# Performance work log

Hardware: AMD Instinct MI355X
Metric: run time of the kernel (lower is better)

Reference implementation:

```python
import jax, jax.numpy as jnp
import numpy as np

N, E = 50000, 800000
IN_DIM, H, OUT = 16, 256, 64
L = 3
REL_DIM, ROLE_DIM, COL_DIM = 16, 8, 8
NUM_REL, NUM_ROLE, NUM_COL = 8, 8, 3
EDGE_IN = 2 * H + REL_DIM + 2 * ROLE_DIM + 2 * COL_DIM   # 560
NODE_IN = 2 * H + ROLE_DIM + COL_DIM                     # 528
LN_EPS = 1e-5


def setup_inputs() -> dict:
    key = jax.random.key(0)
    ks = jax.random.split(key, 32)
    s = 0.02
    inp = {
        "scalars": jax.random.normal(ks[0], (N, IN_DIM), jnp.float32),
        "edge_index": jax.random.randint(ks[1], (2, E), 0, N),
        "edge_relation": jax.random.randint(ks[2], (E,), 0, NUM_REL),
        "node_color_rep": jax.random.randint(ks[3], (N,), 0, NUM_COL),
        "node_role": jax.random.randint(ks[4], (N,), 0, NUM_ROLE),
        # block-level embeddings + input projection (weights stored [in,out])
        "blk_role_emb": jax.random.normal(ks[5], (NUM_ROLE, 8), jnp.float32) * s,
        "blk_color_emb": jax.random.normal(ks[6], (NUM_COL, 8), jnp.float32) * s,
        "in_w": jax.random.normal(ks[7], (IN_DIM + 16, H), jnp.float32) * s,
        "in_b": jnp.zeros((H,), jnp.float32),
        # per-layer params, stacked over L
        "rel_embs": jax.random.normal(ks[8], (L, NUM_REL, REL_DIM), jnp.float32) * s,
        "role_embs": jax.random.normal(ks[9], (L, NUM_ROLE, ROLE_DIM), jnp.float32) * s,
        "col_embs": jax.random.normal(ks[10], (L, NUM_COL, COL_DIM), jnp.float32) * s,
        "e1_w": jax.random.normal(ks[11], (L, EDGE_IN, H), jnp.float32) * s,
        "e1_b": jnp.zeros((L, H), jnp.float32),
        "e2_w": jax.random.normal(ks[12], (L, H, H), jnp.float32) * s,
        "e2_b": jnp.zeros((L, H), jnp.float32),
        "n1_w": jax.random.normal(ks[13], (L, NODE_IN, H), jnp.float32) * s,
        "n1_b": jnp.zeros((L, H), jnp.float32),
        "n2_w": jax.random.normal(ks[14], (L, H, H), jnp.float32) * s,
        "n2_b": jnp.zeros((L, H), jnp.float32),
        "ln_g": jnp.ones((L, H), jnp.float32),
        "ln_b": jnp.zeros((L, H), jnp.float32),
        "out_w": jax.random.normal(ks[15], (H, OUT), jnp.float32) * s,
        "out_b": jnp.zeros((OUT,), jnp.float32),
    }
    return inp


def _layer(h, edge_index, edge_relation, node_color_rep, node_role,
           rel_e, role_e, col_e, e1w, e1b, e2w, e2b, n1w, n1b, n2w, n2b, g, b):
    src, dst = edge_index[0], edge_index[1]
    role_all = role_e[node_role]           # [N, ROLE_DIM]
    col_all = col_e[node_color_rep]        # [N, COL_DIM]
    edge_in = jnp.concatenate(
        [h[src], h[dst], rel_e[edge_relation],
         role_all[src], role_all[dst], col_all[src], col_all[dst]], axis=-1)
    m = jax.nn.silu(edge_in @ e1w + e1b)
    m = jax.nn.silu(m @ e2w + e2b)                       # [E, H]
    agg = jax.ops.segment_sum(m, dst, num_segments=h.shape[0])
    node_in = jnp.concatenate([h, agg, role_all, col_all], axis=-1)
    upd = jax.nn.silu(node_in @ n1w + n1b) @ n2w + n2b
    x = h + upd
    mu = jnp.mean(x, axis=-1, keepdims=True)
    var = jnp.mean(jnp.square(x - mu), axis=-1, keepdims=True)
    return g * (x - mu) * jax.lax.rsqrt(var + LN_EPS) + b


def reference(scalars, edge_index, edge_relation, node_color_rep, node_role,
              blk_role_emb, blk_color_emb, in_w, in_b,
              rel_embs, role_embs, col_embs,
              e1_w, e1_b, e2_w, e2_b, n1_w, n1_b, n2_w, n2_b,
              ln_g, ln_b, out_w, out_b):
    node_in = jnp.concatenate(
        [scalars, blk_color_emb[node_color_rep], blk_role_emb[node_role]], axis=-1)
    h = node_in @ in_w + in_b
    for i in range(L):
        h = _layer(h, edge_index, edge_relation, node_color_rep, node_role,
                   rel_embs[i], role_embs[i], col_embs[i],
                   e1_w[i], e1_b[i], e2_w[i], e2_b[i],
                   n1_w[i], n1_b[i], n2_w[i], n2_b[i],
                   ln_g[i], ln_b[i])
    return h @ out_w + out_b
```

## Files before the change

### kernel.cpp

```cpp
#include <hip/hip_runtime.h>

#define NN 50000
#define NE 800000
#define H 256
#define NBINS 50176

typedef __bf16 bf16x8 __attribute__((ext_vector_type(8)));
typedef __bf16 bf16x4 __attribute__((ext_vector_type(4)));
typedef float f32x4 __attribute__((ext_vector_type(4)));

static __device__ __forceinline__ f32x4 mfma16(bf16x8 a, bf16x8 b, f32x4 c) {
  return __builtin_amdgcn_mfma_f32_16x16x32_bf16(a, b, c, 0, 0, 0);
}
static __device__ __forceinline__ bf16x8 bzero8() {
  bf16x8 z;
#pragma unroll
  for (int j = 0; j < 8; ++j) z[j] = (__bf16)0.f;
  return z;
}
static __device__ __forceinline__ float silu_f(float v) {
  return v * __builtin_amdgcn_rcpf(1.f + __builtin_amdgcn_exp2f(v * -1.442695041f));
}

__global__ void prep_kernel(
    const float* __restrict__ e1w, const float* __restrict__ e2w,
    const float* __restrict__ n1w, const float* __restrict__ n2w,
    const float* __restrict__ outw,
    __bf16* __restrict__ wsd, __bf16* __restrict__ e2p,
    __bf16* __restrict__ n1p, __bf16* __restrict__ n2p,
    __bf16* __restrict__ outp)
{
  int i = blockIdx.x * 256 + threadIdx.x;
  if (i < 3 * 131072) {
    const int l = i / 131072, rem = i % 131072;
    const int c = rem >> 14, r2 = rem & 16383;
    const int n = r2 >> 5, k = c * 32 + (r2 & 31);
    wsd[i] = (n < 256) ? (__bf16)e1w[((size_t)l * 560 + k) * 256 + n]
                       : (__bf16)e1w[((size_t)l * 560 + 256 + k) * 256 + (n - 256)];
    return;
  }
  i -= 3 * 131072;
  if (i < 3 * 8 * 8192) {
    const int l = i / 65536, rem = i % 65536;
    const int c = rem >> 13, r2 = rem & 8191;
    const int n = r2 >> 5, k = c * 32 + (r2 & 31);
    e2p[i] = (__bf16)e2w[((size_t)l * 256 + k) * 256 + n];
    return;
  }
  i -= 3 * 8 * 8192;
  if (i < 3 * 17 * 8192) {
    const int l = i / (17 * 8192), rem = i % (17 * 8192);
    const int c = rem >> 13, r2 = rem & 8191;
    const int n = r2 >> 5, k = c * 32 + (r2 & 31);
    n1p[i] = (k < 528) ? (__bf16)n1w[((size_t)l * 528 + k) * 256 + n] : (__bf16)0.f;
    return;
  }
  i -= 3 * 17 * 8192;
  if (i < 3 * 8 * 8192) {
    const int l = i / 65536, rem = i % 65536;
    const int c = rem >> 13, r2 = rem & 8191;
    const int n = r2 >> 5, k = c * 32 + (r2 & 31);
    n2p[i] = (__bf16)n2w[((size_t)l * 256 + k) * 256 + n];
    return;
  }
  i -= 3 * 8 * 8192;
  if (i < 8 * 2048) {
    const int c = i >> 11, r2 = i & 2047;
    const int n = r2 >> 5, k = c * 32 + (r2 & 31);
    outp[i] = (__bf16)outw[(size_t)k * 64 + n];
  }
}

__global__ __launch_bounds__(256) void tbl_kernel(
    const float* __restrict__ e1w, const float* __restrict__ e1b,
    const float* __restrict__ rel_embs, const float* __restrict__ role_embs,
    const float* __restrict__ col_embs,
    float* __restrict__ TR, float* __restrict__ TS, float* __restrict__ TD)
{
  const int l = blockIdx.x, c = threadIdx.x;
  float w[48];
#pragma unroll
  for (int j = 0; j < 48; ++j) w[j] = e1w[((size_t)l * 560 + 512 + j) * 256 + c];
#pragma unroll
  for (int r = 0; r < 8; ++r) {
    float s = 0.f;
#pragma unroll
    for (int j = 0; j < 16; ++j) s += rel_embs[l * 128 + r * 16 + j] * w[j];
    TR[((size_t)l * 8 + r) * 256 + c] = s;
  }
  const float bias = e1b[l * 256 + c];
#pragma unroll
  for (int ro = 0; ro < 8; ++ro) {
    float ss = 0.f, sd = 0.f;
#pragma unroll
    for (int j = 0; j < 8; ++j) {
      ss += role_embs[l * 64 + ro * 8 + j] * w[16 + j];
      sd += role_embs[l * 64 + ro * 8 + j] * w[24 + j];
    }
#pragma unroll
    for (int co = 0; co < 3; ++co) {
      float cs = 0.f, cd = 0.f;
#pragma unroll
      for (int j = 0; j < 8; ++j) {
        cs += col_embs[l * 24 + co * 8 + j] * w[32 + j];
        cd += col_embs[l * 24 + co * 8 + j] * w[40 + j];
      }
      TS[((size_t)l * 24 + ro * 3 + co) * 256 + c] = ss + cs;
      TD[((size_t)l * 24 + ro * 3 + co) * 256 + c] = sd + cd + bias;
    }
  }
}

__global__ void hist_kernel(const int* __restrict__ dstI, int* __restrict__ cnt) {
  const int e = blockIdx.x * 256 + threadIdx.x;
  if (e < NE) atomicAdd(&cnt[dstI[e]], 1);
}

__global__ __launch_bounds__(256) void scan_kernel(int* __restrict__ cnt) {
  __shared__ int wsum[4];
  __shared__ int sCarry;
  const int tid = threadIdx.x, lane = tid & 63, wid = tid >> 6;
  if (tid == 0) sCarry = 0;
  __syncthreads();
  for (int base = 0; base < NBINS; base += 256) {
    const int i = base + tid;
    const int v = cnt[i];
    int x = v;
#pragma unroll
    for (int d = 1; d < 64; d <<= 1) {
      const int y = __shfl_up(x, d, 64);
      if (lane >= d) x += y;
    }
    if (lane == 63) wsum[wid] = x;
    __syncthreads();
    int wpref = 0;
#pragma unroll
    for (int w = 0; w < 4; ++w)
      if (w < wid) wpref += wsum[w];
    cnt[i] = sCarry + wpref + x - v;
    __syncthreads();
    if (tid == 0) sCarry += wsum[0] + wsum[1] + wsum[2] + wsum[3];
    __syncthreads();
  }
}

__global__ void scatter_kernel(const int* __restrict__ srcI, const int* __restrict__ dstI,
                               const int* __restrict__ erel, int* __restrict__ cnt,
                               int* __restrict__ srcS, int* __restrict__ dstS,
                               int* __restrict__ relS) {
  const int e = blockIdx.x * 256 + threadIdx.x;
  if (e < NE) {
    const int d = dstI[e];
    const int pos = atomicAdd(&cnt[d], 1);
    srcS[pos] = srcI[e];
    dstS[pos] = d;
    relS[pos] = erel[e];
  }
}

__global__ __launch_bounds__(256) void embed_kernel(
    const float* __restrict__ scalars, const int* __restrict__ ncol,
    const int* __restrict__ nrole,
    const float* __restrict__ colEmb, const float* __restrict__ roleEmb,
    const float* __restrict__ inw, const float* __restrict__ inb,
    __bf16* __restrict__ h)
{
  __shared__ float sW[32][256];
  __shared__ float sIn[16][32];
  const int tid = threadIdx.x;
  const int n0 = blockIdx.x * 16;
#pragma unroll
  for (int j = 0; j < 32; ++j) sW[j][tid] = inw[j * 256 + tid];
  {
    const int node = tid >> 4, k = tid & 15;
    const int n = n0 + node;
    sIn[node][k] = (n < NN) ? scalars[(size_t)n * 16 + k] : 0.f;
  }
  if (tid < 16) {
    const int n = n0 + tid;
    if (n < NN) {
      const int c = ncol[n], r = nrole[n];
#pragma unroll
      for (int j = 0; j < 8; ++j) {
        sIn[tid][16 + j] = colEmb[c * 8 + j];
        sIn[tid][24 + j] = roleEmb[r * 8 + j];
      }
    } else {
#pragma unroll
      for (int j = 0; j < 16; ++j) sIn[tid][16 + j] = 0.f;
    }
  }
  __syncthreads();
  const float bias = inb[tid];
  for (int nn = 0; nn < 16; ++nn) {
    const int n = n0 + nn;
    if (n >= NN) break;
    float acc = bias;
#pragma unroll
    for (int k = 0; k < 32; ++k) acc += sIn[nn][k] * sW[k][tid];
    h[(size_t)n * H + tid] = (__bf16)acc;
  }
}

__global__ __launch_bounds__(256, 4) void pre_kernel(
    const __bf16* __restrict__ h, const int* __restrict__ nrole,
    const int* __restrict__ ncol, const __bf16* __restrict__ wsd,
    const float* __restrict__ TS, const float* __restrict__ TD,
    __bf16* __restrict__ PS, __bf16* __restrict__ PD)
{
  __shared__ __align__(16) __bf16 Ah[64][72];
  const int tid  = threadIdx.x;
  const int lane = tid & 63;
  const int wave = tid >> 6;
  const int l15  = lane & 15;
  const int quad = lane >> 4;
  const int n0   = (blockIdx.x >> 1) * 64;
  const int half = blockIdx.x & 1;
  const int colW = wave * 64;

  f32x4 acc[4][4] = {};
  for (int s = 0; s < 4; ++s) {
    if (s) __syncthreads();
#pragma unroll
    for (int it = 0; it < 2; ++it) {
      const int t = tid + it * 256;
      const int row = t >> 3, seg = t & 7;
      const int n = n0 + row;
      bf16x8 v = bzero8();
      if (n < NN) v = *(const bf16x8*)(h + (size_t)n * H + s * 64 + seg * 8);
      *(bf16x8*)&Ah[row][seg * 8] = v;
    }
    __syncthreads();
#pragma unroll
    for (int cc = 0; cc < 2; ++cc) {
      const int c = 2 * s + cc;
      bf16x8 bfr[4], afr[4];
#pragma unroll
      for (int nj = 0; nj < 4; ++nj)
        bfr[nj] = *(const bf16x8*)(wsd + ((size_t)c * 512 + half * 256 + colW + nj * 16 + l15) * 32 + quad * 8);
#pragma unroll
      for (int mi = 0; mi < 4; ++mi)
        afr[mi] = *(const bf16x8*)&Ah[mi * 16 + l15][cc * 32 + quad * 8];
#pragma unroll
      for (int mi = 0; mi < 4; ++mi)
#pragma unroll
        for (int nj = 0; nj < 4; ++nj)
          acc[mi][nj] = mfma16(afr[mi], bfr[nj], acc[mi][nj]);
    }
  }

  const float* T = half ? TD : TS;
  __bf16* P = half ? PD : PS;
#pragma unroll
  for (int mi = 0; mi < 4; ++mi)
#pragma unroll
    for (int r = 0; r < 4; ++r) {
      const int n = n0 + mi * 16 + quad * 4 + r;
      if (n < NN) {
        const int ti = (nrole[n] * 3 + ncol[n]) * 256;
#pragma unroll
        for (int nj = 0; nj < 4; ++nj) {
          const int col = colW + nj * 16 + l15;
          P[(size_t)n * H + col] = (__bf16)(acc[mi][nj][r] + T[ti + col]);
        }
      }
    }
}

__global__ __launch_bounds__(256, 4) void edge_kernel(
    const __bf16* __restrict__ PS, const __bf16* __restrict__ PD,
    float* __restrict__ agg,
    const int* __restrict__ srcS, const int* __restrict__ dstS,
    const int* __restrict__ relS, const float* __restrict__ TR,
    const __bf16* __restrict__ e2p, const float* __restrict__ e2b)
{
  __shared__ __align__(16) char uni[34816];
  __shared__ __bf16 sTrel[8][256];
  __shared__ int sSrc[64], sDst[64], sRel[64];
  __shared__ int sFlag[2];

  auto A2  = (__bf16 (*)[264])uni;
  auto A2t = (__bf16 (*)[68])uni;

  const int tid  = threadIdx.x;
  const int lane = tid & 63;
  const int wave = tid >> 6;
  const int l15  = lane & 15;
  const int quad = lane >> 4;
  const int e0   = blockIdx.x * 64;
  const int colW = wave * 64;

  if (tid < 64) {
    sSrc[tid] = srcS[e0 + tid];
    sDst[tid] = dstS[e0 + tid];
    sRel[tid] = relS[e0 + tid];
  }
  {
    const int r = tid >> 5, cs = (tid & 31) * 8;
    const float* p = TR + r * 256 + cs;
    bf16x8 v;
#pragma unroll
    for (int j = 0; j < 8; ++j) v[j] = (__bf16)p[j];
    *(bf16x8*)&sTrel[r][cs] = v;
  }
  if (tid == 0) sFlag[0] = (e0 > 0) && (dstS[e0 - 1] == dstS[e0]);
  if (tid == 1) sFlag[1] = (e0 + 64 < NE) && (dstS[e0 + 64] == dstS[e0 + 63]);
  __syncthreads();

  {
    const int brow = tid >> 5;
    const int cs = (tid & 31) * 8;
#pragma unroll
    for (int it = 0; it < 8; ++it) {
      const int row = it * 8 + brow;
      const bf16x8 a = *(const bf16x8*)(PS + (size_t)sSrc[row] * H + cs);
      const bf16x8 b = *(const bf16x8*)(PD + (size_t)sDst[row] * H + cs);
      const bf16x8 t = *(const bf16x8*)&sTrel[sRel[row]][cs];
      bf16x8 o;
#pragma unroll
      for (int j = 0; j < 8; ++j)
        o[j] = (__bf16)silu_f((float)a[j] + (float)b[j] + (float)t[j]);
      *(bf16x8*)&A2[row][cs] = o;
    }
  }
  __syncthreads();

  f32x4 acc2[4][4] = {};
#pragma unroll
  for (int c = 0; c < 8; ++c) {
    bf16x8 bfr[4], afr[4];
#pragma unroll
    for (int nj = 0; nj < 4; ++nj)
      bfr[nj] = *(const bf16x8*)(e2p + ((size_t)c * 256 + colW + nj * 16 + l15) * 32 + quad * 8);
#pragma unroll
    for (int mi = 0; mi < 4; ++mi)
      afr[mi] = *(const bf16x8*)&A2[mi * 16 + l15][c * 32 + quad * 8];
#pragma unroll
    for (int mi = 0; mi < 4; ++mi)
#pragma unroll
      for (int nj = 0; nj < 4; ++nj)
        acc2[mi][nj] = mfma16(afr[mi], bfr[nj], acc2[mi][nj]);
  }

  float b2[4];
#pragma unroll
  for (int nj = 0; nj < 4; ++nj) b2[nj] = e2b[colW + nj * 16 + l15];
  __syncthreads();

#pragma unroll
  for (int mi = 0; mi < 4; ++mi)
#pragma unroll
    for (int nj = 0; nj < 4; ++nj) {
      const int col = colW + nj * 16 + l15;
      bf16x4 pv;
#pragma unroll
      for (int r = 0; r < 4; ++r)
        pv[r] = (__bf16)silu_f(acc2[mi][nj][r] + b2[nj]);
      *(bf16x4*)&A2t[col][mi * 16 + quad * 4] = pv;
    }
  __syncthreads();

  {
    const int col = tid;
    const bool f = (lane > 0) && (sDst[lane] != sDst[lane - 1]);
    const unsigned long long mask = __ballot(f);
    const bool fF = sFlag[0] != 0, fL = sFlag[1] != 0;
    bf16x4 v[16];
#pragma unroll
    for (int j = 0; j < 16; ++j) v[j] = *(const bf16x4*)&A2t[col][j * 4];
    float sum = 0.f;
    int s0 = 0;
#pragma unroll
    for (int r = 0; r < 64; ++r) {
      sum += (float)v[r >> 2][r & 3];
      if (r == 63 || ((mask >> (r + 1)) & 1ull)) {
        float* addr = agg + (size_t)sDst[r] * H + col;
        const bool shared = (s0 == 0 && fF) || (r == 63 && fL);
        if (shared) atomicAdd(addr, sum);
        else *addr = sum;
        sum = 0.f;
        s0 = r + 1;
      }
    }
  }
}

__global__ __launch_bounds__(256, 4) void node_kernel(
    __bf16* __restrict__ h, const float* __restrict__ agg,
    const int* __restrict__ nrole, const int* __restrict__ ncol,
    const float* __restrict__ roleE, const float* __restrict__ colE,
    const __bf16* __restrict__ n1p, const float* __restrict__ n1b,
    const __bf16* __restrict__ n2p, const float* __restrict__ n2b,
    const float* __restrict__ lng, const float* __restrict__ lnb)
{
  __shared__ __align__(16) char uni[33792];
  __shared__ __bf16 sRole[8][8], sCol[3][8];
  __shared__ float sSum[64][4], sSsq[64][4];

  auto Abuf = (__bf16 (*)[72])uni;
  auto A2   = (__bf16 (*)[264])uni;

  const int tid  = threadIdx.x;
  const int lane = tid & 63;
  const int wave = tid >> 6;
  const int l15  = lane & 15;
  const int quad = lane >> 4;
  const int n0   = blockIdx.x * 64;
  const int colW = wave * 64;

  if (tid < 64) ((__bf16*)sRole)[tid] = (__bf16)roleE[tid];
  else if (tid < 88) ((__bf16*)sCol)[tid - 64] = (__bf16)colE[tid - 64];
  __syncthreads();

  f32x4 acc[4][4] = {};
  for (int s = 0; s < 9; ++s) {
    if (s) __syncthreads();
    if (s < 4) {
#pragma unroll
      for (int it = 0; it < 2; ++it) {
        const int t = tid + it * 256;
        const int row = t >> 3, seg = t & 7;
        const int n = n0 + row;
        bf16x8 v = bzero8();
        if (n < NN) v = *(const bf16x8*)(h + (size_t)n * H + s * 64 + seg * 8);
        *(bf16x8*)&Abuf[row][seg * 8] = v;
      }
    } else if (s < 8) {
#pragma unroll
      for (int it = 0; it < 2; ++it) {
        const int t = tid + it * 256;
        const int row = t >> 3, seg = t & 7;
        const int n = n0 + row;
        bf16x8 v = bzero8();
        if (n < NN) {
          const float* p = agg + (size_t)n * H + (s - 4) * 64 + seg * 8;
          const float4 u0 = *(const float4*)p;
          const float4 u1 = *(const float4*)(p + 4);
          v[0] = (__bf16)u0.x; v[1] = (__bf16)u0.y; v[2] = (__bf16)u0.z; v[3] = (__bf16)u0.w;
          v[4] = (__bf16)u1.x; v[5] = (__bf16)u1.y; v[6] = (__bf16)u1.z; v[7] = (__bf16)u1.w;
        }
        *(bf16x8*)&Abuf[row][seg * 8] = v;
      }
    } else {
      const int row = tid >> 2, q = tid & 3;
      const int n = n0 + row;
      __bf16* dp = &Abuf[row][q * 16];
      if (q == 0 && n < NN) {
        const int r = nrole[n], c = ncol[n];
#pragma unroll
        for (int j = 0; j < 8; ++j) { dp[j] = sRole[r][j]; dp[8 + j] = sCol[c][j]; }
      } else {
#pragma unroll
        for (int j = 0; j < 16; ++j) dp[j] = (__bf16)0.f;
      }
    }
    __syncthreads();
#pragma unroll
    for (int cc = 0; cc < 2; ++cc) {
      const int c = 2 * s + cc;
      if (c >= 17) break;
      bf16x8 bfr[4], afr[4];
#pragma unroll
      for (int nj = 0; nj < 4; ++nj)
        bfr[nj] = *(const bf16x8*)(n1p + ((size_t)c * 256 + colW + nj * 16 + l15) * 32 + quad * 8);
#pragma unroll
      for (int mi = 0; mi < 4; ++mi)
        afr[mi] = *(const bf16x8*)&Abuf[mi * 16 + l15][cc * 32 + quad * 8];
#pragma unroll
      for (int mi = 0; mi < 4; ++mi)
#pragma unroll
        for (int nj = 0; nj < 4; ++nj)
          acc[mi][nj] = mfma16(afr[mi], bfr[nj], acc[mi][nj]);
    }
  }
  __syncthreads();

  float b1[4];
#pragma unroll
  for (int nj = 0; nj < 4; ++nj) b1[nj] = n1b[colW + nj * 16 + l15];
#pragma unroll
  for (int mi = 0; mi < 4; ++mi)
#pragma unroll
    for (int nj = 0; nj < 4; ++nj)
#pragma unroll
      for (int r = 0; r < 4; ++r)
        A2[mi * 16 + quad * 4 + r][colW + nj * 16 + l15] =
            (__bf16)silu_f(acc[mi][nj][r] + b1[nj]);
  __syncthreads();

  f32x4 acc2[4][4] = {};
#pragma unroll
  for (int c = 0; c < 8; ++c) {
    bf16x8 bfr[4], afr[4];
#pragma unroll
    for (int nj = 0; nj < 4; ++nj)
      bfr[nj] = *(const bf16x8*)(n2p + ((size_t)c * 256 + colW + nj * 16 + l15) * 32 + quad * 8);
#pragma unroll
    for (int mi = 0; mi < 4; ++mi)
      afr[mi] = *(const bf16x8*)&A2[mi * 16 + l15][c * 32 + quad * 8];
#pragma unroll
    for (int mi = 0; mi < 4; ++mi)
#pragma unroll
      for (int nj = 0; nj < 4; ++nj)
        acc2[mi][nj] = mfma16(afr[mi], bfr[nj], acc2[mi][nj]);
  }

  float b2[4], g4[4], bb4[4];
#pragma unroll
  for (int nj = 0; nj < 4; ++nj) {
    const int col = colW + nj * 16 + l15;
    b2[nj] = n2b[col]; g4[nj] = lng[col]; bb4[nj] = lnb[col];
  }
#pragma unroll
  for (int mi = 0; mi < 4; ++mi)
#pragma unroll
    for (int r = 0; r < 4; ++r) {
      const int n = n0 + mi * 16 + quad * 4 + r;
#pragma unroll
      for (int nj = 0; nj < 4; ++nj) {
        const float hv = (n < NN) ? (float)h[(size_t)n * H + colW + nj * 16 + l15] : 0.f;
        acc2[mi][nj][r] += b2[nj] + hv;
      }
    }
#pragma unroll
  for (int mi = 0; mi < 4; ++mi)
#pragma unroll
    for (int r = 0; r < 4; ++r) {
      float s1 = 0.f, s2 = 0.f;
#pragma unroll
      for (int nj = 0; nj < 4; ++nj) {
        const float v = acc2[mi][nj][r];
        s1 += v; s2 += v * v;
      }
#pragma unroll
      for (int d = 1; d < 16; d <<= 1) {
        s1 += __shfl_xor(s1, d, 16);
        s2 += __shfl_xor(s2, d, 16);
      }
      if (l15 == 0) {
        const int row = mi * 16 + quad * 4 + r;
        sSum[row][wave] = s1; sSsq[row][wave] = s2;
      }
    }
  __syncthreads();
#pragma unroll
  for (int mi = 0; mi < 4; ++mi)
#pragma unroll
    for (int r = 0; r < 4; ++r) {
      const int row = mi * 16 + quad * 4 + r;
      const int n = n0 + row;
      const float t1 = sSum[row][0] + sSum[row][1] + sSum[row][2] + sSum[row][3];
      const float t2 = sSsq[row][0] + sSsq[row][1] + sSsq[row][2] + sSsq[row][3];
      const float mu = t1 * (1.f / 256.f);
      float var = t2 * (1.f / 256.f) - mu * mu;
      var = var < 0.f ? 0.f : var;
      const float rstd = rsqrtf(var + 1e-5f);
      if (n < NN) {
#pragma unroll
        for (int nj = 0; nj < 4; ++nj) {
          const float o = g4[nj] * (acc2[mi][nj][r] - mu) * rstd + bb4[nj];
          h[(size_t)n * H + colW + nj * 16 + l15] = (__bf16)o;
        }
      }
    }
}

__global__ __launch_bounds__(256) void out_kernel(
    const __bf16* __restrict__ h, const __bf16* __restrict__ outp,
    const float* __restrict__ outb, float* __restrict__ out)
{
  const int tid  = threadIdx.x;
  const int lane = tid & 63;
  const int wave = tid >> 6;
  const int l15  = lane & 15;
  const int quad = lane >> 4;
  const int m0   = blockIdx.x * 64 + wave * 16;
  int ar = m0 + l15;
  if (ar >= NN) ar = NN - 1;
  f32x4 acc[4] = {};
#pragma unroll
  for (int c = 0; c < 8; ++c) {
    const bf16x8 a = *(const bf16x8*)(h + (size_t)ar * H + c * 32 + quad * 8);
#pragma unroll
    for (int nj = 0; nj < 4; ++nj) {
      const bf16x8 b = *(const bf16x8*)(outp + ((size_t)c * 64 + nj * 16 + l15) * 32 + quad * 8);
      acc[nj] = mfma16(a, b, acc[nj]);
    }
  }
#pragma unroll
  for (int nj = 0; nj < 4; ++nj) {
    const float bb = outb[nj * 16 + l15];
#pragma unroll
    for (int r = 0; r < 4; ++r) {
      const int row = m0 + quad * 4 + r;
      if (row < NN) out[(size_t)row * 64 + nj * 16 + l15] = acc[nj][r] + bb;
    }
  }
}

extern "C" void kernel_launch(void* const* d_in, const int* in_sizes, int n_in,
                              void* d_out, int out_size, void* d_ws, size_t ws_size,
                              hipStream_t stream) {
  const float* scalars   = (const float*)d_in[0];
  const int*   ei        = (const int*)d_in[1];
  const int*   erel      = (const int*)d_in[2];
  const int*   ncol      = (const int*)d_in[3];
  const int*   nrole     = (const int*)d_in[4];
  const float* blk_role  = (const float*)d_in[5];
  const float* blk_col   = (const float*)d_in[6];
  const float* inw       = (const float*)d_in[7];
  const float* inb       = (const float*)d_in[8];
  const float* rel_embs  = (const float*)d_in[9];
  const float* role_embs = (const float*)d_in[10];
  const float* col_embs  = (const float*)d_in[11];
  const float* e1w       = (const float*)d_in[12];
  const float* e1b       = (const float*)d_in[13];
  const float* e2w       = (const float*)d_in[14];
  const float* e2b       = (const float*)d_in[15];
  const float* n1w       = (const float*)d_in[16];
  const float* n1b       = (const float*)d_in[17];
  const float* n2w       = (const float*)d_in[18];
  const float* n2b       = (const float*)d_in[19];
  const float* lng       = (const float*)d_in[20];
  const float* lnb       = (const float*)d_in[21];
  const float* outw      = (const float*)d_in[22];
  const float* outb      = (const float*)d_in[23];

  const int* srcI = ei;
  const int* dstI = ei + NE;

  char* ws = (char*)d_ws;
  size_t off = 0;
  auto take = [&](size_t bytes) -> char* {
    off = (off + 255) & ~(size_t)255;
    char* p = ws + off;
    off += bytes;
    return p;
  };
  __bf16* h    = (__bf16*)take((size_t)NN * H * 2);
  float*  agg  = (float*)take((size_t)NN * H * 4);
  __bf16* PS   = (__bf16*)take((size_t)NN * H * 2);
  __bf16* PD   = (__bf16*)take((size_t)NN * H * 2);
  __bf16* wsd  = (__bf16*)take((size_t)3 * 131072 * 2);
  __bf16* e2p  = (__bf16*)take((size_t)3 * 8 * 8192 * 2);
  __bf16* n1p  = (__bf16*)take((size_t)3 * 17 * 8192 * 2);
  __bf16* n2p  = (__bf16*)take((size_t)3 * 8 * 8192 * 2);
  __bf16* outp = (__bf16*)take((size_t)8 * 2048 * 2);
  float*  TR   = (float*)take((size_t)3 * 8 * 256 * 4);
  float*  TS   = (float*)take((size_t)3 * 24 * 256 * 4);
  float*  TD   = (float*)take((size_t)3 * 24 * 256 * 4);
  int*    cnt  = (int*)take((size_t)NBINS * 4);
  int*    srcS = (int*)take((size_t)NE * 4);
  int*    dstS = (int*)take((size_t)NE * 4);
  int*    relS = (int*)take((size_t)NE * 4);

  prep_kernel<<<4768, 256, 0, stream>>>(e1w, e2w, n1w, n2w, outw,
                                        wsd, e2p, n1p, n2p, outp);
  tbl_kernel<<<3, 256, 0, stream>>>(e1w, e1b, rel_embs, role_embs, col_embs,
                                    TR, TS, TD);
  embed_kernel<<<(NN + 15) / 16, 256, 0, stream>>>(scalars, ncol, nrole,
                                                   blk_col, blk_role, inw, inb, h);
  hipMemsetAsync(cnt, 0, (size_t)NBINS * 4, stream);
  hist_kernel<<<(NE + 255) / 256, 256, 0, stream>>>(dstI, cnt);
  scan_kernel<<<1, 256, 0, stream>>>(cnt);
  scatter_kernel<<<(NE + 255) / 256, 256, 0, stream>>>(srcI, dstI, erel, cnt,
                                                       srcS, dstS, relS);

  for (int l = 0; l < 3; ++l) {
    hipMemsetAsync(agg, 0, (size_t)NN * H * 4, stream);
    pre_kernel<<<2 * ((NN + 63) / 64), 256, 0, stream>>>(
        h, nrole, ncol, wsd + (size_t)l * 131072,
        TS + (size_t)l * 24 * 256, TD + (size_t)l * 24 * 256, PS, PD);
    edge_kernel<<<NE / 64, 256, 0, stream>>>(
        PS, PD, agg, srcS, dstS, relS, TR + (size_t)l * 8 * 256,
        e2p + (size_t)l * 8 * 8192, e2b + (size_t)l * 256);
    node_kernel<<<(NN + 63) / 64, 256, 0, stream>>>(
        h, agg, nrole, ncol,
        role_embs + (size_t)l * 64, col_embs + (size_t)l * 24,
        n1p + (size_t)l * 17 * 8192, n1b + (size_t)l * 256,
        n2p + (size_t)l * 8 * 8192,  n2b + (size_t)l * 256,
        lng + (size_t)l * 256, lnb + (size_t)l * 256);
  }
  out_kernel<<<(NN + 63) / 64, 256, 0, stream>>>(h, outp, outb, (float*)d_out);
}
```

Baseline: 1.297 ms.

## Fuse next-layer projection and output head into node kernel, drop agg memset and atomics

Several changes at once. The next layer's PS/PD projection and the final output projection are fused into the node kernel, which removes the per-layer pre_kernel and the out_kernel. Edge blocks now write their boundary partial sums to a separate bnd buffer instead of using atomics, and the node kernel reduces those partials using CSR offsets. This removes the per-layer agg memset and the atomicAdd traffic. The tbl kernel and the cnt zeroing are merged into prep, the scan is widened to 1024 threads with int4 loads, and src and rel are packed into one int array (src assumes fewer than 65536 nodes). In exchange the node kernel carries more registers and more complex aggregation reads.

```diff
diff --git a/kernel.cpp b/kernel.cpp
--- a/kernel.cpp
+++ b/kernel.cpp
@@ -3,6 +3,7 @@
 #define NN 50000
 #define NE 800000
 #define H 256
+#define NB (NE / 64)
 #define NBINS 50176
 
 typedef __bf16 bf16x8 __attribute__((ext_vector_type(8)));
@@ -21,14 +22,20 @@
 static __device__ __forceinline__ float silu_f(float v) {
   return v * __builtin_amdgcn_rcpf(1.f + __builtin_amdgcn_exp2f(v * -1.442695041f));
 }
+static __device__ __forceinline__ void add4(float4& a, const float4 b) {
+  a.x += b.x; a.y += b.y; a.z += b.z; a.w += b.w;
+}
 
 __global__ void prep_kernel(
     const float* __restrict__ e1w, const float* __restrict__ e2w,
     const float* __restrict__ n1w, const float* __restrict__ n2w,
-    const float* __restrict__ outw,
+    const float* __restrict__ outw, const float* __restrict__ e1b,
+    const float* __restrict__ rel_embs, const float* __restrict__ role_embs,
+    const float* __restrict__ col_embs,
     __bf16* __restrict__ wsd, __bf16* __restrict__ e2p,
     __bf16* __restrict__ n1p, __bf16* __restrict__ n2p,
-    __bf16* __restrict__ outp)
+    __bf16* __restrict__ outp, int* __restrict__ cnt,
+    float* __restrict__ TR, float* __restrict__ TS, float* __restrict__ TD)
 {
   int i = blockIdx.x * 256 + threadIdx.x;
   if (i < 3 * 131072) {
@@ -40,73 +47,71 @@
     return;
   }
   i -= 3 * 131072;
-  if (i < 3 * 8 * 8192) {
+  if (i < 3 * 65536) {
     const int l = i / 65536, rem = i % 65536;
     const int c = rem >> 13, r2 = rem & 8191;
     const int n = r2 >> 5, k = c * 32 + (r2 & 31);
     e2p[i] = (__bf16)e2w[((size_t)l * 256 + k) * 256 + n];
     return;
   }
-  i -= 3 * 8 * 8192;
-  if (i < 3 * 17 * 8192) {
-    const int l = i / (17 * 8192), rem = i % (17 * 8192);
+  i -= 3 * 65536;
+  if (i < 3 * 139264) {
+    const int l = i / 139264, rem = i % 139264;
     const int c = rem >> 13, r2 = rem & 8191;
     const int n = r2 >> 5, k = c * 32 + (r2 & 31);
     n1p[i] = (k < 528) ? (__bf16)n1w[((size_t)l * 528 + k) * 256 + n] : (__bf16)0.f;
     return;
   }
-  i -= 3 * 17 * 8192;
-  if (i < 3 * 8 * 8192) {
+  i -= 3 * 139264;
+  if (i < 3 * 65536) {
     const int l = i / 65536, rem = i % 65536;
     const int c = rem >> 13, r2 = rem & 8191;
     const int n = r2 >> 5, k = c * 32 + (r2 & 31);
     n2p[i] = (__bf16)n2w[((size_t)l * 256 + k) * 256 + n];
     return;
   }
-  i -= 3 * 8 * 8192;
-  if (i < 8 * 2048) {
+  i -= 3 * 65536;
+  if (i < 16384) {
     const int c = i >> 11, r2 = i & 2047;
     const int n = r2 >> 5, k = c * 32 + (r2 & 31);
     outp[i] = (__bf16)outw[(size_t)k * 64 + n];
-  }
-}
-
-__global__ __launch_bounds__(256) void tbl_kernel(
-    const float* __restrict__ e1w, const float* __restrict__ e1b,
-    const float* __restrict__ rel_embs, const float* __restrict__ role_embs,
-    const float* __restrict__ col_embs,
-    float* __restrict__ TR, float* __restrict__ TS, float* __restrict__ TD)
-{
-  const int l = blockIdx.x, c = threadIdx.x;
-  float w[48];
-#pragma unroll
-  for (int j = 0; j < 48; ++j) w[j] = e1w[((size_t)l * 560 + 512 + j) * 256 + c];
-#pragma unroll
-  for (int r = 0; r < 8; ++r) {
-    float s = 0.f;
-#pragma unroll
-    for (int j = 0; j < 16; ++j) s += rel_embs[l * 128 + r * 16 + j] * w[j];
-    TR[((size_t)l * 8 + r) * 256 + c] = s;
-  }
-  const float bias = e1b[l * 256 + c];
-#pragma unroll
-  for (int ro = 0; ro < 8; ++ro) {
-    float ss = 0.f, sd = 0.f;
-#pragma unroll
-    for (int j = 0; j < 8; ++j) {
-      ss += role_embs[l * 64 + ro * 8 + j] * w[16 + j];
-      sd += role_embs[l * 64 + ro * 8 + j] * w[24 + j];
-    }
-#pragma unroll
-    for (int co = 0; co < 3; ++co) {
-      float cs = 0.f, cd = 0.f;
+    return;
+  }
+  i -= 16384;
+  if (i < NBINS) { cnt[i] = 0; return; }
+  i -= NBINS;
+  if (i < 768) {
+    const int l = i >> 8, c = i & 255;
+    float w[48];
+#pragma unroll
+    for (int j = 0; j < 48; ++j) w[j] = e1w[((size_t)l * 560 + 512 + j) * 256 + c];
+#pragma unroll
+    for (int r = 0; r < 8; ++r) {
+      float s = 0.f;
+#pragma unroll
+      for (int j = 0; j < 16; ++j) s += rel_embs[l * 128 + r * 16 + j] * w[j];
+      TR[((size_t)l * 8 + r) * 256 + c] = s;
+    }
+    const float bias = e1b[l * 256 + c];
+#pragma unroll
+    for (int ro = 0; ro < 8; ++ro) {
+      float ss = 0.f, sd = 0.f;
 #pragma unroll
       for (int j = 0; j < 8; ++j) {
-        cs += col_embs[l * 24 + co * 8 + j] * w[32 + j];
-        cd += col_embs[l * 24 + co * 8 + j] * w[40 + j];
-      }
-      TS[((size_t)l * 24 + ro * 3 + co) * 256 + c] = ss + cs;
-      TD[((size_t)l * 24 + ro * 3 + co) * 256 + c] = sd + cd + bias;
+        ss += role_embs[l * 64 + ro * 8 + j] * w[16 + j];
+        sd += role_embs[l * 64 + ro * 8 + j] * w[24 + j];
+      }
+#pragma unroll
+      for (int co = 0; co < 3; ++co) {
+        float cs = 0.f, cd = 0.f;
+#pragma unroll
+        for (int j = 0; j < 8; ++j) {
+          cs += col_embs[l * 24 + co * 8 + j] * w[32 + j];
+          cd += col_embs[l * 24 + co * 8 + j] * w[40 + j];
+        }
+        TS[((size_t)l * 24 + ro * 3 + co) * 256 + c] = ss + cs;
+        TD[((size_t)l * 24 + ro * 3 + co) * 256 + c] = sd + cd + bias;
+      }
     }
   }
 }
@@ -116,16 +121,18 @@
   if (e < NE) atomicAdd(&cnt[dstI[e]], 1);
 }
 
-__global__ __launch_bounds__(256) void scan_kernel(int* __restrict__ cnt) {
-  __shared__ int wsum[4];
-  __shared__ int sCarry;
+__global__ __launch_bounds__(1024) void scan_kernel(int* __restrict__ cnt) {
+  __shared__ int wsum[16];
+  __shared__ int carry;
   const int tid = threadIdx.x, lane = tid & 63, wid = tid >> 6;
-  if (tid == 0) sCarry = 0;
-  __syncthreads();
-  for (int base = 0; base < NBINS; base += 256) {
-    const int i = base + tid;
-    const int v = cnt[i];
-    int x = v;
+  if (tid == 0) carry = 0;
+  __syncthreads();
+  for (int base = 0; base < NBINS; base += 4096) {
+    const int idx = base + tid * 4;
+    int4 v = make_int4(0, 0, 0, 0);
+    if (idx < NBINS) v = *(const int4*)&cnt[idx];
+    const int s1 = v.x + v.y, s2 = s1 + v.z, tot = s2 + v.w;
+    int x = tot;
 #pragma unroll
     for (int d = 1; d < 64; d <<= 1) {
       const int y = __shfl_up(x, d, 64);
@@ -135,26 +142,34 @@
     __syncthreads();
     int wpref = 0;
 #pragma unroll
-    for (int w = 0; w < 4; ++w)
+    for (int w = 0; w < 16; ++w)
       if (w < wid) wpref += wsum[w];
-    cnt[i] = sCarry + wpref + x - v;
+    const int ex = carry + wpref + (x - tot);
+    if (idx < NBINS) {
+      int4 o;
+      o.x = ex; o.y = ex + v.x; o.z = ex + s1; o.w = ex + s2;
+      *(int4*)&cnt[idx] = o;
+    }
     __syncthreads();
-    if (tid == 0) sCarry += wsum[0] + wsum[1] + wsum[2] + wsum[3];
+    if (tid == 0) {
+      int s = 0;
+#pragma unroll
+      for (int w = 0; w < 16; ++w) s += wsum[w];
+      carry += s;
+    }
     __syncthreads();
   }
 }
 
 __global__ void scatter_kernel(const int* __restrict__ srcI, const int* __restrict__ dstI,
                                const int* __restrict__ erel, int* __restrict__ cnt,
-                               int* __restrict__ srcS, int* __restrict__ dstS,
-                               int* __restrict__ relS) {
+                               int* __restrict__ esr, int* __restrict__ dstS) {
   const int e = blockIdx.x * 256 + threadIdx.x;
   if (e < NE) {
     const int d = dstI[e];
     const int pos = atomicAdd(&cnt[d], 1);
-    srcS[pos] = srcI[e];
+    esr[pos] = srcI[e] | (erel[e] << 16);
     dstS[pos] = d;
-    relS[pos] = erel[e];
   }
 }
 
@@ -269,15 +284,14 @@
 
 __global__ __launch_bounds__(256, 4) void edge_kernel(
     const __bf16* __restrict__ PS, const __bf16* __restrict__ PD,
-    float* __restrict__ agg,
-    const int* __restrict__ srcS, const int* __restrict__ dstS,
-    const int* __restrict__ relS, const float* __restrict__ TR,
+    float* __restrict__ agg, float* __restrict__ bnd,
+    const int* __restrict__ esr, const int* __restrict__ dstS,
+    const float* __restrict__ TR,
     const __bf16* __restrict__ e2p, const float* __restrict__ e2b)
 {
   __shared__ __align__(16) char uni[34816];
   __shared__ __bf16 sTrel[8][256];
   __shared__ int sSrc[64], sDst[64], sRel[64];
-  __shared__ int sFlag[2];
 
   auto A2  = (__bf16 (*)[264])uni;
   auto A2t = (__bf16 (*)[68])uni;
@@ -291,9 +305,10 @@
   const int colW = wave * 64;
 
   if (tid < 64) {
-    sSrc[tid] = srcS[e0 + tid];
+    const int u = esr[e0 + tid];
+    sSrc[tid] = u & 0xffff;
+    sRel[tid] = u >> 16;
     sDst[tid] = dstS[e0 + tid];
-    sRel[tid] = relS[e0 + tid];
   }
   {
     const int r = tid >> 5, cs = (tid & 31) * 8;
@@ -303,8 +318,6 @@
     for (int j = 0; j < 8; ++j) v[j] = (__bf16)p[j];
     *(bf16x8*)&sTrel[r][cs] = v;
   }
-  if (tid == 0) sFlag[0] = (e0 > 0) && (dstS[e0 - 1] == dstS[e0]);
-  if (tid == 1) sFlag[1] = (e0 + 64 < NE) && (dstS[e0 + 64] == dstS[e0 + 63]);
   __syncthreads();
 
   {
@@ -364,20 +377,25 @@
     const int col = tid;
     const bool f = (lane > 0) && (sDst[lane] != sDst[lane - 1]);
     const unsigned long long mask = __ballot(f);
-    const bool fF = sFlag[0] != 0, fL = sFlag[1] != 0;
     bf16x4 v[16];
 #pragma unroll
     for (int j = 0; j < 16; ++j) v[j] = *(const bf16x4*)&A2t[col][j * 4];
+    float* bnd0 = bnd + ((size_t)2 * blockIdx.x) * 256 + col;
     float sum = 0.f;
     int s0 = 0;
 #pragma unroll
     for (int r = 0; r < 64; ++r) {
       sum += (float)v[r >> 2][r & 3];
       if (r == 63 || ((mask >> (r + 1)) & 1ull)) {
-        float* addr = agg + (size_t)sDst[r] * H + col;
-        const bool shared = (s0 == 0 && fF) || (r == 63 && fL);
-        if (shared) atomicAdd(addr, sum);
-        else *addr = sum;
+        const bool isFirst = (s0 == 0), isLast = (r == 63);
+        if (isFirst) {
+          bnd0[0] = isLast ? 0.f : sum;
+          if (isLast) bnd0[256] = sum;
+        } else if (isLast) {
+          bnd0[256] = sum;
+        } else {
+          agg[(size_t)sDst[r] * H + col] = sum;
+        }
         sum = 0.f;
         s0 = r + 1;
       }
@@ -387,15 +405,22 @@
 
 __global__ __launch_bounds__(256, 4) void node_kernel(
     __bf16* __restrict__ h, const float* __restrict__ agg,
+    const float* __restrict__ bnd, const int* __restrict__ cnt,
     const int* __restrict__ nrole, const int* __restrict__ ncol,
     const float* __restrict__ roleE, const float* __restrict__ colE,
     const __bf16* __restrict__ n1p, const float* __restrict__ n1b,
     const __bf16* __restrict__ n2p, const float* __restrict__ n2b,
-    const float* __restrict__ lng, const float* __restrict__ lnb)
+    const float* __restrict__ lng, const float* __restrict__ lnb,
+    const int mode,
+    const __bf16* __restrict__ wsdN, const float* __restrict__ TSn,
+    const float* __restrict__ TDn, __bf16* __restrict__ PS, __bf16* __restrict__ PD,
+    const __bf16* __restrict__ outp, const float* __restrict__ outb,
+    float* __restrict__ out)
 {
   __shared__ __align__(16) char uni[33792];
   __shared__ __bf16 sRole[8][8], sCol[3][8];
   __shared__ float sSum[64][4], sSsq[64][4];
+  __shared__ int sStart[64], sEnd[64], sTi[64];
 
   auto Abuf = (__bf16 (*)[72])uni;
   auto A2   = (__bf16 (*)[264])uni;
@@ -408,8 +433,19 @@
   const int n0   = blockIdx.x * 64;
   const int colW = wave * 64;
 
-  if (tid < 64) ((__bf16*)sRole)[tid] = (__bf16)roleE[tid];
-  else if (tid < 88) ((__bf16*)sCol)[tid - 64] = (__bf16)colE[tid - 64];
+  if (tid < 64) {
+    const int n = n0 + tid;
+    int st = 0, en = 0, ti = 0;
+    if (n < NN) {
+      st = (n > 0) ? cnt[n - 1] : 0;
+      en = cnt[n];
+      ti = (nrole[n] * 3 + ncol[n]) * 256;
+    }
+    sStart[tid] = st; sEnd[tid] = en; sTi[tid] = ti;
+    ((__bf16*)sRole)[tid] = (__bf16)roleE[tid];
+  } else if (tid < 88) {
+    ((__bf16*)sCol)[tid - 64] = (__bf16)colE[tid - 64];
+  }
   __syncthreads();
 
   f32x4 acc[4][4] = {};
@@ -430,15 +466,35 @@
       for (int it = 0; it < 2; ++it) {
         const int t = tid + it * 256;
         const int row = t >> 3, seg = t & 7;
-        const int n = n0 + row;
-        bf16x8 v = bzero8();
-        if (n < NN) {
-          const float* p = agg + (size_t)n * H + (s - 4) * 64 + seg * 8;
-          const float4 u0 = *(const float4*)p;
-          const float4 u1 = *(const float4*)(p + 4);
-          v[0] = (__bf16)u0.x; v[1] = (__bf16)u0.y; v[2] = (__bf16)u0.z; v[3] = (__bf16)u0.w;
-          v[4] = (__bf16)u1.x; v[5] = (__bf16)u1.y; v[6] = (__bf16)u1.z; v[7] = (__bf16)u1.w;
+        const int off = (s - 4) * 64 + seg * 8;
+        const int st = sStart[row], en = sEnd[row];
+        float4 u0 = make_float4(0.f, 0.f, 0.f, 0.f);
+        float4 u1 = make_float4(0.f, 0.f, 0.f, 0.f);
+        if (en > st) {
+          const int bs = st >> 6, be = (en - 1) >> 6;
+          const bool interior = (bs == be) && (st & 63) != 0 && (en & 63) != 0;
+          if (interior) {
+            const float* p = agg + (size_t)(n0 + row) * H + off;
+            u0 = *(const float4*)p;
+            u1 = *(const float4*)(p + 4);
+          } else {
+            for (int b = bs; b <= be; ++b) {
+              if (b > bs || (st & 63) == 0) {
+                const float* p = bnd + ((size_t)2 * b) * 256 + off;
+                add4(u0, *(const float4*)p);
+                add4(u1, *(const float4*)(p + 4));
+              }
+              if (b < be || (en & 63) == 0) {
+                const float* p = bnd + ((size_t)2 * b + 1) * 256 + off;
+                add4(u0, *(const float4*)p);
+                add4(u1, *(const float4*)(p + 4));
+              }
+            }
+          }
         }
+        bf16x8 v;
+        v[0] = (__bf16)u0.x; v[1] = (__bf16)u0.y; v[2] = (__bf16)u0.z; v[3] = (__bf16)u0.w;
+        v[4] = (__bf16)u1.x; v[5] = (__bf16)u1.y; v[6] = (__bf16)u1.z; v[7] = (__bf16)u1.w;
         *(bf16x8*)&Abuf[row][seg * 8] = v;
       }
     } else {
@@ -543,6 +599,7 @@
       }
     }
   __syncthreads();
+
 #pragma unroll
   for (int mi = 0; mi < 4; ++mi)
 #pragma unroll
@@ -555,46 +612,72 @@
       float var = t2 * (1.f / 256.f) - mu * mu;
       var = var < 0.f ? 0.f : var;
       const float rstd = rsqrtf(var + 1e-5f);
-      if (n < NN) {
-#pragma unroll
-        for (int nj = 0; nj < 4; ++nj) {
-          const float o = g4[nj] * (acc2[mi][nj][r] - mu) * rstd + bb4[nj];
-          h[(size_t)n * H + colW + nj * 16 + l15] = (__bf16)o;
+#pragma unroll
+      for (int nj = 0; nj < 4; ++nj) {
+        const int col = colW + nj * 16 + l15;
+        const float o = g4[nj] * (acc2[mi][nj][r] - mu) * rstd + bb4[nj];
+        const __bf16 ob = (__bf16)o;
+        A2[row][col] = ob;
+        if (mode == 0 && n < NN) h[(size_t)n * H + col] = ob;
+      }
+    }
+  __syncthreads();
+
+  if (mode == 0) {
+    for (int hf = 0; hf < 2; ++hf) {
+      f32x4 ap[4][4] = {};
+#pragma unroll
+      for (int c = 0; c < 8; ++c) {
+        bf16x8 bfr[4], afr[4];
+#pragma unroll
+        for (int nj = 0; nj < 4; ++nj)
+          bfr[nj] = *(const bf16x8*)(wsdN + ((size_t)c * 512 + hf * 256 + colW + nj * 16 + l15) * 32 + quad * 8);
+#pragma unroll
+        for (int mi = 0; mi < 4; ++mi)
+          afr[mi] = *(const bf16x8*)&A2[mi * 16 + l15][c * 32 + quad * 8];
+#pragma unroll
+        for (int mi = 0; mi < 4; ++mi)
+#pragma unroll
+          for (int nj = 0; nj < 4; ++nj)
+            ap[mi][nj] = mfma16(afr[mi], bfr[nj], ap[mi][nj]);
+      }
+      const float* T = hf ? TDn : TSn;
+      __bf16* P = hf ? PD : PS;
+#pragma unroll
+      for (int mi = 0; mi < 4; ++mi)
+#pragma unroll
+        for (int r = 0; r < 4; ++r) {
+          const int row = mi * 16 + quad * 4 + r;
+          const int n = n0 + row;
+          if (n < NN) {
+            const int ti = sTi[row];
+#pragma unroll
+            for (int nj = 0; nj < 4; ++nj) {
+              const int col = colW + nj * 16 + l15;
+              P[(size_t)n * H + col] = (__bf16)(ap[mi][nj][r] + T[ti + col]);
+            }
+          }
         }
-      }
-    }
-}
-
-__global__ __launch_bounds__(256) void out_kernel(
-    const __bf16* __restrict__ h, const __bf16* __restrict__ outp,
-    const float* __restrict__ outb, float* __restrict__ out)
-{
-  const int tid  = threadIdx.x;
-  const int lane = tid & 63;
-  const int wave = tid >> 6;
-  const int l15  = lane & 15;
-  const int quad = lane >> 4;
-  const int m0   = blockIdx.x * 64 + wave * 16;
-  int ar = m0 + l15;
-  if (ar >= NN) ar = NN - 1;
-  f32x4 acc[4] = {};
-#pragma unroll
-  for (int c = 0; c < 8; ++c) {
-    const bf16x8 a = *(const bf16x8*)(h + (size_t)ar * H + c * 32 + quad * 8);
-#pragma unroll
-    for (int nj = 0; nj < 4; ++nj) {
-      const bf16x8 b = *(const bf16x8*)(outp + ((size_t)c * 64 + nj * 16 + l15) * 32 + quad * 8);
-      acc[nj] = mfma16(a, b, acc[nj]);
-    }
-  }
-#pragma unroll
-  for (int nj = 0; nj < 4; ++nj) {
-    const float bb = outb[nj * 16 + l15];
-#pragma unroll
-    for (int r = 0; r < 4; ++r) {
-      const int row = m0 + quad * 4 + r;
-      if (row < NN) out[(size_t)row * 64 + nj * 16 + l15] = acc[nj][r] + bb;
-    }
+    }
+  } else {
+    f32x4 ao[4] = {};
+#pragma unroll
+    for (int c = 0; c < 8; ++c) {
+      const bf16x8 bfr = *(const bf16x8*)(outp + ((size_t)c * 64 + wave * 16 + l15) * 32 + quad * 8);
+#pragma unroll
+      for (int mi = 0; mi < 4; ++mi) {
+        const bf16x8 afr = *(const bf16x8*)&A2[mi * 16 + l15][c * 32 + quad * 8];
+        ao[mi] = mfma16(afr, bfr, ao[mi]);
+      }
+    }
+    const float ob = outb[wave * 16 + l15];
+#pragma unroll
+    for (int mi = 0; mi < 4; ++mi)
+#pragma unroll
+      for (int r = 0; r < 4; ++r) {
+        const int n = n0 + mi * 16 + quad * 4 + r;
+        if (n < NN) out[(size_t)n * 64 + wave * 16 + l15] = ao[mi][r] + ob;
+      }
   }
 }
 
@@ -639,47 +722,48 @@
   };
   __bf16* h    = (__bf16*)take((size_t)NN * H * 2);
   float*  agg  = (float*)take((size_t)NN * H * 4);
+  float*  bnd  = (float*)take((size_t)2 * NB * 256 * 4);
   __bf16* PS   = (__bf16*)take((size_t)NN * H * 2);
   __bf16* PD   = (__bf16*)take((size_t)NN * H * 2);
   __bf16* wsd  = (__bf16*)take((size_t)3 * 131072 * 2);
-  __bf16* e2p  = (__bf16*)take((size_t)3 * 8 * 8192 * 2);
-  __bf16* n1p  = (__bf16*)take((size_t)3 * 17 * 8192 * 2);
-  __bf16* n2p  = (__bf16*)take((size_t)3 * 8 * 8192 * 2);
-  __bf16* outp = (__bf16*)take((size_t)8 * 2048 * 2);
+  __bf16* e2p  = (__bf16*)take((size_t)3 * 65536 * 2);
+  __bf16* n1p  = (__bf16*)take((size_t)3 * 139264 * 2);
+  __bf16* n2p  = (__bf16*)take((size_t)3 * 65536 * 2);
+  __bf16* outp = (__bf16*)take((size_t)16384 * 2);
   float*  TR   = (float*)take((size_t)3 * 8 * 256 * 4);
   float*  TS   = (float*)take((size_t)3 * 24 * 256 * 4);
   float*  TD   = (float*)take((size_t)3 * 24 * 256 * 4);
   int*    cnt  = (int*)take((size_t)NBINS * 4);
-  int*    srcS = (int*)take((size_t)NE * 4);
+  int*    esr  = (int*)take((size_t)NE * 4);
   int*    dstS = (int*)take((size_t)NE * 4);
-  int*    relS = (int*)take((size_t)NE * 4);
-
-  prep_kernel<<<4768, 256, 0, stream>>>(e1w, e2w, n1w, n2w, outw,
-                                        wsd, e2p, n1p, n2p, outp);
-  tbl_kernel<<<3, 256, 0, stream>>>(e1w, e1b, rel_embs, role_embs, col_embs,
-                                    TR, TS, TD);
+
+  prep_kernel<<<4967, 256, 0, stream>>>(e1w, e2w, n1w, n2w, outw, e1b,
+                                        rel_embs, role_embs, col_embs,
+                                        wsd, e2p, n1p, n2p, outp, cnt, TR, TS, TD);
+  hist_kernel<<<(NE + 255) / 256, 256, 0, stream>>>(dstI, cnt);
+  scan_kernel<<<1, 1024, 0, stream>>>(cnt);
+  scatter_kernel<<<(NE + 255) / 256, 256, 0, stream>>>(srcI, dstI, erel, cnt,
+                                                       esr, dstS);
   embed_kernel<<<(NN + 15) / 16, 256, 0, stream>>>(scalars, ncol, nrole,
                                                    blk_col, blk_role, inw, inb, h);
-  hipMemsetAsync(cnt, 0, (size_t)NBINS * 4, stream);
-  hist_kernel<<<(NE + 255) / 256, 256, 0, stream>>>(dstI, cnt);
-  scan_kernel<<<1, 256, 0, stream>>>(cnt);
-  scatter_kernel<<<(NE + 255) / 256, 256, 0, stream>>>(srcI, dstI, erel, cnt,
-                                                       srcS, dstS, relS);
+  pre_kernel<<<2 * ((NN + 63) / 64), 256, 0, stream>>>(
+      h, nrole, ncol, wsd, TS, TD, PS, PD);
 
   for (int l = 0; l < 3; ++l) {
-    hipMemsetAsync(agg, 0, (size_t)NN * H * 4, stream);
-    pre_kernel<<<2 * ((NN + 63) / 64), 256, 0, stream>>>(
-        h, nrole, ncol, wsd + (size_t)l * 131072,
-        TS + (size_t)l * 24 * 256, TD + (size_t)l * 24 * 256, PS, PD);
-    edge_kernel<<<NE / 64, 256, 0, stream>>>(
-        PS, PD, agg, srcS, dstS, relS, TR + (size_t)l * 8 * 256,
-        e2p + (size_t)l * 8 * 8192, e2b + (size_t)l * 256);
+    edge_kernel<<<NB, 256, 0, stream>>>(
+        PS, PD, agg, bnd, esr, dstS, TR + (size_t)l * 2048,
+        e2p + (size_t)l * 65536, e2b + (size_t)l * 256);
+    const int mode = (l < 2) ? 0 : 1;
     node_kernel<<<(NN + 63) / 64, 256, 0, stream>>>(
-        h, agg, nrole, ncol,
+        h, agg, bnd, cnt, nrole, ncol,
         role_embs + (size_t)l * 64, col_embs + (size_t)l * 24,
-        n1p + (size_t)l * 17 * 8192, n1b + (size_t)l * 256,
-        n2p + (size_t)l * 8 * 8192,  n2b + (size_t)l * 256,
-        lng + (size_t)l * 256, lnb + (size_t)l * 256);
-  }
-  out_kernel<<<(NN + 63) / 64, 256, 0, stream>>>(h, outp, outb, (float*)d_out);
-}
+        n1p + (size_t)l * 139264, n1b + (size_t)l * 256,
+        n2p + (size_t)l * 65536,  n2b + (size_t)l * 256,
+        lng + (size_t)l * 256, lnb + (size_t)l * 256,
+        mode,
+        wsd + (size_t)(l + 1 < 3 ? l + 1 : 0) * 131072,
+        TS + (size_t)(l + 1 < 3 ? l + 1 : 0) * 6144,
+        TD + (size_t)(l + 1 < 3 ? l + 1 : 0) * 6144,
+        PS, PD, outp, outb, (float*)d_out);
+  }
+}
```

Result: no change. 1.308 ms (+0.9%).
